# Performance work log

Measured on AMD Instinct MI355X. Metric: run time of the kernel, lower is better.

Reference implementation:

```python
import jax, jax.numpy as jnp
import numpy as np

N_HEAD, D_MODEL, D_HEAD = 16, 1024, 64
SEQ, BSZ = 2048, 4
LN_EPS = 1e-5
SCALE = 1.0 / D_HEAD ** 0.5


def layer_norm(x, gamma, beta):
    m = jnp.mean(x, axis=-1, keepdims=True)
    v = jnp.mean(jnp.square(x - m), axis=-1, keepdims=True)
    return (x - m) * jax.lax.rsqrt(v + LN_EPS) * gamma + beta


def setup_inputs() -> dict:
    key = jax.random.key(0)
    k1, k2, k3, k4, k5, k6 = jax.random.split(key, 6)
    h = jax.random.normal(k1, (SEQ, BSZ, D_MODEL), dtype=jnp.float32)
    attn_mask = jax.random.bernoulli(k2, 0.1, (SEQ, BSZ))
    s = 1.0 / np.sqrt(D_MODEL)
    Wq = jax.random.normal(k3, (D_MODEL, N_HEAD * D_HEAD), dtype=jnp.float32) * s
    Wkv = jax.random.normal(k4, (D_MODEL, 2 * N_HEAD * D_HEAD), dtype=jnp.float32) * s
    Wo = jax.random.normal(k5, (N_HEAD * D_HEAD, D_MODEL), dtype=jnp.float32) * s
    gamma = jnp.ones((D_MODEL,), dtype=jnp.float32)
    beta = jnp.zeros((D_MODEL,), dtype=jnp.float32)
    return {"h": h, "attn_mask": attn_mask, "Wq": Wq, "Wkv": Wkv,
            "Wo": Wo, "gamma": gamma, "beta": beta}


def reference(h, attn_mask, Wq, Wkv, Wo, gamma, beta):
    # h: [S, B, D]; post-LN variant (pre_lnorm=False), mems=None so c == h
    S, B, _ = h.shape
    head_q = (h @ Wq).reshape(S, B, N_HEAD, D_HEAD)
    kv = h @ Wkv
    head_k, head_v = jnp.split(kv, 2, axis=-1)
    head_k = head_k.reshape(S, B, N_HEAD, D_HEAD)
    head_v = head_v.reshape(S, B, N_HEAD, D_HEAD)
    # scores [qlen, klen, B, n]
    attn_score = jnp.einsum('ibnd,jbnd->ijbn', head_q, head_k) * SCALE
    # 2D mask [klen, B] broadcast as [1, klen, B, 1]
    attn_score = jnp.where(attn_mask[None, :, :, None], -jnp.inf, attn_score)
    attn_prob = jax.nn.softmax(attn_score, axis=1)
    attn_vec = jnp.einsum('ijbn,jbnd->ibnd', attn_prob, head_v)
    attn_vec = attn_vec.reshape(S, B, N_HEAD * D_HEAD)
    attn_out = attn_vec @ Wo
    return layer_norm(h + attn_out, gamma, beta)
```

## Files before the change

### kernel.cpp

```cpp
#include <hip/hip_runtime.h>
#include <stdint.h>

#define SEQ 2048
#define BSZ 4
#define NHEAD 16
#define DHEAD 64
#define DMODEL 1024
#define NHD (NHEAD * DHEAD)
#define KVSTR (2 * NHD)

typedef unsigned short u16;
typedef unsigned char u8;
typedef unsigned int u32;
typedef float v4f __attribute__((ext_vector_type(4)));
typedef short v8s __attribute__((ext_vector_type(8)));
typedef u32 v4u __attribute__((ext_vector_type(4)));
typedef u32 v2u __attribute__((ext_vector_type(2)));

#define MASK_NEG 30000.0f
#define BF16_ONES_PAIR 0x3F803F80u

__device__ __forceinline__ float bf2f(u16 h) { return __uint_as_float(((u32)h) << 16); }
__device__ __forceinline__ u16 f2bf(float f) {
  u32 u = __float_as_uint(f);
  return (u16)((u + 0x7fffu + ((u >> 16) & 1u)) >> 16);
}
__device__ __forceinline__ v4f v4f_zero() {
  v4f z; z[0] = 0.f; z[1] = 0.f; z[2] = 0.f; z[3] = 0.f; return z;
}
__device__ __forceinline__ bool is_bf16_mode(const u32* gprobe) {
  return *gprobe == BF16_ONES_PAIR;
}
__device__ __forceinline__ u32 pack_bf16_trunc(float a, float b) {
  return __builtin_amdgcn_perm(__float_as_uint(b), __float_as_uint(a), 0x07060302u);
}

typedef __attribute__((address_space(3))) u32 lds_u32_t;
typedef const __attribute__((address_space(1))) u32 g_u32_t;
__device__ __forceinline__ void async_cp16(const u16* gp, u16* lp) {
  __builtin_amdgcn_global_load_lds((g_u32_t*)gp, (lds_u32_t*)lp, 16, 0, 0);
}

__global__ __launch_bounds__(256) void cast_h(
    const void* __restrict__ src, const u32* __restrict__ gprobe,
    u16* __restrict__ dst) {
  bool bf = is_bf16_mode(gprobe);
  int i4 = blockIdx.x * 256 + threadIdx.x;
  if (bf) {
    ((v2u*)dst)[i4] = ((const v2u*)src)[i4];
  } else {
    v4f v = ((const v4f*)src)[i4];
    v2u o;
    o[0] = (u32)f2bf(v[0]) | ((u32)f2bf(v[1]) << 16);
    o[1] = (u32)f2bf(v[2]) | ((u32)f2bf(v[3]) << 16);
    ((v2u*)dst)[i4] = o;
  }
}

__global__ __launch_bounds__(256) void transpose_w3(
    const void* __restrict__ Wq, const void* __restrict__ Wkv,
    const void* __restrict__ Wo, const u32* __restrict__ gprobe,
    const u32* __restrict__ mraw,
    u16* __restrict__ WqT, u16* __restrict__ WkvT, u16* __restrict__ WoT,
    float* __restrict__ maskf) {
  int z = blockIdx.z;
  if (z == 3) {
    int flat = blockIdx.y * 64 + blockIdx.x;
    if (flat >= 32) return;
    bool int8mode = false;
    for (int i = 0; i < 64; ++i) {
      u32 v = mraw[i];
      if (v != 0u && v != 1u && v != 0x3F800000u) int8mode = true;
    }
    int idx = flat * 256 + threadIdx.x;
    int b = idx >> 11, j = idx & 2047;
    u32 val = int8mode ? (u32)((const u8*)mraw)[j * BSZ + b] : mraw[j * BSZ + b];
    maskf[idx] = val ? -MASK_NEG : 0.0f;
    return;
  }
  bool bf = is_bf16_mode(gprobe);
  int C = (z == 1) ? 2048 : 1024;
  if (blockIdx.x * 32 >= (unsigned)C) return;
  const void* src = (z == 0) ? Wq : (z == 1) ? Wkv : Wo;
  u16* outp = (z == 0) ? WqT : (z == 1) ? WkvT : WoT;
  __shared__ u16 tile[32][33];
  int c0 = blockIdx.x * 32, r0 = blockIdx.y * 32;
  int tx = threadIdx.x & 31, ty = threadIdx.x >> 5;
  if (bf) {
    const u16* in = (const u16*)src;
#pragma unroll
    for (int rr = 0; rr < 4; ++rr)
      tile[ty + rr * 8][tx] = in[(r0 + ty + rr * 8) * C + c0 + tx];
  } else {
    const float* in = (const float*)src;
#pragma unroll
    for (int rr = 0; rr < 4; ++rr)
      tile[ty + rr * 8][tx] = f2bf(in[(r0 + ty + rr * 8) * C + c0 + tx]);
  }
  __syncthreads();
#pragma unroll
  for (int rr = 0; rr < 4; ++rr)
    outp[(c0 + ty + rr * 8) * 1024 + r0 + tx] = tile[tx][ty + rr * 8];
}

__global__ __launch_bounds__(256) void build_vt(
    const u16* __restrict__ KV, u16* __restrict__ Vt) {
  __shared__ u16 tile[32][33];
  int bn = blockIdx.z;
  int b = bn >> 4, n = bn & 15;
  int s0 = blockIdx.x * 32, d0 = blockIdx.y * 32;
  int tx = threadIdx.x & 31, ty = threadIdx.x >> 5;
#pragma unroll
  for (int rr = 0; rr < 4; ++rr) {
    int s = s0 + ty + rr * 8;
    tile[ty + rr * 8][tx] = KV[(s * BSZ + b) * KVSTR + NHD + n * DHEAD + d0 + tx];
  }
  __syncthreads();
  const int ptx = ((tx >> 2) & 3) * 8 + ((tx >> 4) & 1) * 4 + (tx & 3);
#pragma unroll
  for (int rr = 0; rr < 4; ++rr) {
    int d = d0 + ty + rr * 8;
    Vt[bn * (DHEAD * SEQ) + d * SEQ + s0 + ptx] = tile[tx][ty + rr * 8];
  }
}

__global__ __launch_bounds__(256) void gemm_qkv(
    const u16* __restrict__ A, const u16* __restrict__ Bt,
    u16* __restrict__ Qm, u16* __restrict__ KVm) {
  const int K = 1024;
  __shared__ __align__(16) u16 As[2][128 * 32];
  __shared__ __align__(16) u16 Bs[2][128 * 32];
  const int tid = threadIdx.x;
  const int lane = tid & 63, w = tid >> 6;
  const int quad = lane >> 4, l16 = lane & 15;
  const int wm = w >> 1, wn = w & 1;
  const int flat = blockIdx.y * 24 + blockIdx.x;
  const int xcd = flat & 7, idx = flat >> 3;
  const int m0 = (idx / 3) * 128;
  const int n0 = (xcd * 3 + idx % 3) * 128;
  const int qsw = quad ^ ((l16 >> 1) & 3);

  const int c8 = ((tid & 3) ^ ((tid >> 3) & 3)) * 8;
  const u16* aA = A + (size_t)(m0 + (tid >> 2)) * K + c8;
  const u16* bB = Bt + (size_t)(n0 + (tid >> 2)) * K + c8;

#define QKV_STAGE(bi, kk)                                   \
  do {                                                      \
    async_cp16(aA + (kk), &As[bi][8 * tid]);                \
    async_cp16(aA + 64 * K + (kk), &As[bi][2048 + 8 * tid]);\
    async_cp16(bB + (kk), &Bs[bi][8 * tid]);                \
    async_cp16(bB + 64 * K + (kk), &Bs[bi][2048 + 8 * tid]);\
  } while (0)

  v4f acc[4][4];
#pragma unroll
  for (int i = 0; i < 4; ++i)
#pragma unroll
    for (int j = 0; j < 4; ++j) acc[i][j] = v4f_zero();

  QKV_STAGE(0, 0);
  asm volatile("s_waitcnt vmcnt(0)" ::: "memory");
  __syncthreads();

  for (int k0 = 0; k0 < K; k0 += 32) {
    const int cur = (k0 >> 5) & 1;
    if (k0 + 32 < K) QKV_STAGE(cur ^ 1, k0 + 32);
    const u16* AsC = As[cur];
    const u16* BsC = Bs[cur];
    v8s a[4], b[4];
#pragma unroll
    for (int i = 0; i < 4; ++i)
      a[i] = *(const v8s*)(AsC + (wm * 64 + i * 16 + l16) * 32 + qsw * 8);
#pragma unroll
    for (int j = 0; j < 4; ++j)
      b[j] = *(const v8s*)(BsC + (wn * 64 + j * 16 + l16) * 32 + qsw * 8);
#pragma unroll
    for (int i = 0; i < 4; ++i)
#pragma unroll
      for (int j = 0; j < 4; ++j)
        acc[i][j] = __builtin_amdgcn_mfma_f32_16x16x32_bf16(a[i], b[j], acc[i][j], 0, 0, 0);
    asm volatile("s_waitcnt vmcnt(0)" ::: "memory");
    __syncthreads();
  }
#undef QKV_STAGE
  u16* dst = (n0 < 1024) ? Qm : KVm;
  int stride = (n0 < 1024) ? 1024 : 2048;
  int coff = (n0 < 1024) ? n0 : n0 - 1024;
#pragma unroll
  for (int i = 0; i < 4; ++i)
#pragma unroll
    for (int j = 0; j < 4; ++j)
#pragma unroll
      for (int r = 0; r < 4; ++r) {
        int row = m0 + wm * 64 + i * 16 + quad * 4 + r;
        int col = coff + wn * 64 + j * 16 + l16;
        dst[(size_t)row * stride + col] = f2bf(acc[i][j][r]);
      }
}

__global__ __launch_bounds__(256) void gemm_bt(
    const u16* __restrict__ A, const u16* __restrict__ Bt,
    u16* __restrict__ Cb, float* __restrict__ Cf, int store_f32,
    int N, int K) {
  __shared__ __align__(16) u16 As[2][128 * 32];
  __shared__ __align__(16) u16 Bs[2][128 * 32];
  const int tid = threadIdx.x;
  const int lane = tid & 63, w = tid >> 6;
  const int quad = lane >> 4, l16 = lane & 15;
  const int wm = w >> 1, wn = w & 1;
  const int nbx = gridDim.x;
  const int flat = blockIdx.y * nbx + blockIdx.x;
  const int chunk = (nbx * gridDim.y) >> 3;
  const int logical = (flat & 7) * chunk + (flat >> 3);
  const int m0 = (logical / nbx) * 128, n0 = (logical % nbx) * 128;
  const int qsw = quad ^ ((l16 >> 1) & 3);

  const int c8 = ((tid & 3) ^ ((tid >> 3) & 3)) * 8;
  const u16* aA = A + (size_t)(m0 + (tid >> 2)) * K + c8;
  const u16* bB = Bt + (size_t)(n0 + (tid >> 2)) * K + c8;

#define BT_STAGE(bi, kk)                                    \
  do {                                                      \
    async_cp16(aA + (kk), &As[bi][8 * tid]);                \
    async_cp16(aA + 64 * K + (kk), &As[bi][2048 + 8 * tid]);\
    async_cp16(bB + (kk), &Bs[bi][8 * tid]);                \
    async_cp16(bB + 64 * K + (kk), &Bs[bi][2048 + 8 * tid]);\
  } while (0)

  v4f acc[4][4];
#pragma unroll
  for (int i = 0; i < 4; ++i)
#pragma unroll
    for (int j = 0; j < 4; ++j) acc[i][j] = v4f_zero();

  BT_STAGE(0, 0);
  asm volatile("s_waitcnt vmcnt(0)" ::: "memory");
  __syncthreads();

  for (int k0 = 0; k0 < K; k0 += 32) {
    const int cur = (k0 >> 5) & 1;
    if (k0 + 32 < K) BT_STAGE(cur ^ 1, k0 + 32);
    const u16* AsC = As[cur];
    const u16* BsC = Bs[cur];
    v8s a[4], b[4];
#pragma unroll
    for (int i = 0; i < 4; ++i)
      a[i] = *(const v8s*)(AsC + (wm * 64 + i * 16 + l16) * 32 + qsw * 8);
#pragma unroll
    for (int j = 0; j < 4; ++j)
      b[j] = *(const v8s*)(BsC + (wn * 64 + j * 16 + l16) * 32 + qsw * 8);
#pragma unroll
    for (int i = 0; i < 4; ++i)
#pragma unroll
      for (int j = 0; j < 4; ++j)
        acc[i][j] = __builtin_amdgcn_mfma_f32_16x16x32_bf16(a[i], b[j], acc[i][j], 0, 0, 0);
    asm volatile("s_waitcnt vmcnt(0)" ::: "memory");
    __syncthreads();
  }
#undef BT_STAGE
#pragma unroll
  for (int i = 0; i < 4; ++i)
#pragma unroll
    for (int j = 0; j < 4; ++j)
#pragma unroll
      for (int r = 0; r < 4; ++r) {
        int row = m0 + wm * 64 + i * 16 + quad * 4 + r;
        int col = n0 + wn * 64 + j * 16 + l16;
        if (store_f32) Cf[(size_t)row * N + col] = acc[i][j][r];
        else Cb[(size_t)row * N + col] = f2bf(acc[i][j][r]);
      }
}

__global__ __launch_bounds__(512, 4) void attn(
    const u16* __restrict__ Q, const u16* __restrict__ KV,
    const u16* __restrict__ Vt, const float* __restrict__ maskf,
    u16* __restrict__ AV) {
  __shared__ __align__(16) u16 Ks[2][2 * 64 * 32];
  __shared__ __align__(16) u16 Vs[2][2 * 64 * 32];

  const int tid = threadIdx.x;
  const int lane = tid & 63, w = tid >> 6;
  const int quad = lane >> 4, l16 = lane & 15;
  const int flat = blockIdx.y * 8 + blockIdx.x;
  const int logical = (flat & 7) * 64 + (flat >> 3);
  const int bn = logical >> 3;
  const int b = bn >> 4, n = bn & 15;
  const int q0 = (logical & 7) * 256 + w * 16;
  const int qsw = quad ^ ((l16 >> 1) & 3);

  const float SC = 0.125f * 1.44269504088896340736f;

  const int rl = (tid >> 2) & 63;
  const int half = tid >> 8;
  const int cks = (tid & 3) ^ ((tid >> 3) & 3);
  const u16* kb = KV + ((size_t)rl * BSZ + b) * KVSTR + n * DHEAD + half * 32 + cks * 8;
  const u16* vb = Vt + (size_t)bn * (DHEAD * SEQ) + (size_t)rl * SEQ + half * 32 + cks * 8;

#define STAGE_JT(bi, jtn)                                                  \
  do {                                                                     \
    async_cp16(kb + (size_t)(jtn) * (64 * BSZ * KVSTR), &Ks[bi][8 * tid]); \
    async_cp16(vb + (jtn) * 64,                         &Vs[bi][8 * tid]); \
  } while (0)

  v8s qf[2][2];
#pragma unroll
  for (int s = 0; s < 2; ++s)
#pragma unroll
    for (int c = 0; c < 2; ++c)
      qf[s][c] = *(const v8s*)(Q + ((size_t)(q0 + s * 128 + l16) * BSZ + b) * NHD +
                               n * DHEAD + c * 32 + quad * 8);

  v4f ot[2][4];
#pragma unroll
  for (int s = 0; s < 2; ++s)
#pragma unroll
    for (int d = 0; d < 4; ++d) ot[s][d] = v4f_zero();
  v4f lacc[2];
  lacc[0] = v4f_zero();
  lacc[1] = v4f_zero();
  union OU { v4u u; v8s v; } ones;
  ones.u[0] = BF16_ONES_PAIR; ones.u[1] = BF16_ONES_PAIR;
  ones.u[2] = BF16_ONES_PAIR; ones.u[3] = BF16_ONES_PAIR;

  const float* mrow = maskf + b * SEQ + quad * 4;

  STAGE_JT(0, 0);
  asm volatile("s_waitcnt vmcnt(0)" ::: "memory");
  __syncthreads();

  for (int jt = 0; jt < SEQ / 64; ++jt) {
    const int cur = jt & 1;
    if (jt + 1 < SEQ / 64) STAGE_JT(cur ^ 1, jt + 1);

    v4f mk[4];
#pragma unroll
    for (int t = 0; t < 4; ++t)
      mk[t] = *(const v4f*)(mrow + jt * 64 + t * 16);

    const u16* KsC = Ks[cur];
    const u16* VsC = Vs[cur];

    v4f st[2][4];
    __builtin_amdgcn_s_setprio(1);
#pragma unroll
    for (int t = 0; t < 4; ++t) {
      v8s kf0 = *(const v8s*)(KsC + (t * 16 + l16) * 32 + qsw * 8);
      v8s kf1 = *(const v8s*)(KsC + (2048 + (t * 16 + l16) * 32) + qsw * 8);
#pragma unroll
      for (int s = 0; s < 2; ++s) {
        v4f acc = __builtin_amdgcn_mfma_f32_16x16x32_bf16(kf0, qf[s][0], v4f_zero(), 0, 0, 0);
        st[s][t] = __builtin_amdgcn_mfma_f32_16x16x32_bf16(kf1, qf[s][1], acc, 0, 0, 0);
      }
    }
    __builtin_amdgcn_s_setprio(0);

    union PU { v4u u; v8s s; };
    PU pf[2][2];
#pragma unroll
    for (int s = 0; s < 2; ++s)
#pragma unroll
      for (int t = 0; t < 4; ++t) {
        v4f msk = mk[t];
        float p0 = __builtin_amdgcn_exp2f(fmaf(st[s][t][0], SC, msk[0]));
        float p1 = __builtin_amdgcn_exp2f(fmaf(st[s][t][1], SC, msk[1]));
        float p2 = __builtin_amdgcn_exp2f(fmaf(st[s][t][2], SC, msk[2]));
        float p3 = __builtin_amdgcn_exp2f(fmaf(st[s][t][3], SC, msk[3]));
        pf[s][t >> 1].u[(t & 1) * 2 + 0] = pack_bf16_trunc(p0, p1);
        pf[s][t >> 1].u[(t & 1) * 2 + 1] = pack_bf16_trunc(p2, p3);
      }

    __builtin_amdgcn_s_setprio(1);
#pragma unroll
    for (int tp = 0; tp < 2; ++tp) {
#pragma unroll
      for (int ds = 0; ds < 4; ++ds) {
        v8s vf = *(const v8s*)(VsC + tp * 2048 + (ds * 16 + l16) * 32 + qsw * 8);
#pragma unroll
        for (int s = 0; s < 2; ++s)
          ot[s][ds] = __builtin_amdgcn_mfma_f32_16x16x32_bf16(vf, pf[s][tp].s, ot[s][ds], 0, 0, 0);
      }
#pragma unroll
      for (int s = 0; s < 2; ++s)
        lacc[s] = __builtin_amdgcn_mfma_f32_16x16x32_bf16(ones.v, pf[s][tp].s, lacc[s], 0, 0, 0);
    }
    __builtin_amdgcn_s_setprio(0);

    asm volatile("s_waitcnt vmcnt(0)" ::: "memory");
    __syncthreads();
  }
#undef STAGE_JT

#pragma unroll
  for (int s = 0; s < 2; ++s) {
    float inv = 1.0f / fmaxf(lacc[s][0], 1e-30f);
#pragma unroll
    for (int ds = 0; ds < 4; ++ds)
#pragma unroll
      for (int r = 0; r < 4; ++r) {
        int d = ds * 16 + quad * 4 + r;
        AV[((size_t)(q0 + s * 128 + l16) * BSZ + b) * NHD + n * DHEAD + d] =
            f2bf(ot[s][ds][r] * inv);
      }
  }
}

__global__ __launch_bounds__(256) void add_ln(
    const void* __restrict__ h, const float* __restrict__ AO,
    const void* __restrict__ gamma, const void* __restrict__ beta,
    void* __restrict__ outp) {
  bool bf = is_bf16_mode((const u32*)gamma);
  const int row = blockIdx.x, tid = threadIdx.x;
  const int lane = tid & 63, w = tid >> 6;
  __shared__ float rs1[4], rs2[4];
  const int col = tid * 4;
  v4f av = *(const v4f*)(AO + (size_t)row * DMODEL + col);
  float x[4], g[4], be[4];
  if (bf) {
    v2u hv = ((const v2u*)h)[row * 256 + tid];
    x[0] = bf2f((u16)(hv[0] & 0xffff)) + av[0];
    x[1] = bf2f((u16)(hv[0] >> 16)) + av[1];
    x[2] = bf2f((u16)(hv[1] & 0xffff)) + av[2];
    x[3] = bf2f((u16)(hv[1] >> 16)) + av[3];
    v2u gv = ((const v2u*)gamma)[tid];
    v2u bv = ((const v2u*)beta)[tid];
    g[0] = bf2f((u16)(gv[0] & 0xffff)); g[1] = bf2f((u16)(gv[0] >> 16));
    g[2] = bf2f((u16)(gv[1] & 0xffff)); g[3] = bf2f((u16)(gv[1] >> 16));
    be[0] = bf2f((u16)(bv[0] & 0xffff)); be[1] = bf2f((u16)(bv[0] >> 16));
    be[2] = bf2f((u16)(bv[1] & 0xffff)); be[3] = bf2f((u16)(bv[1] >> 16));
  } else {
    v4f hv = ((const v4f*)h)[row * 256 + tid];
    x[0] = hv[0] + av[0]; x[1] = hv[1] + av[1];
    x[2] = hv[2] + av[2]; x[3] = hv[3] + av[3];
    v4f gv = ((const v4f*)gamma)[tid];
    v4f bv = ((const v4f*)beta)[tid];
    g[0] = gv[0]; g[1] = gv[1]; g[2] = gv[2]; g[3] = gv[3];
    be[0] = bv[0]; be[1] = bv[1]; be[2] = bv[2]; be[3] = bv[3];
  }
  float s1 = x[0] + x[1] + x[2] + x[3];
  float s2 = x[0] * x[0] + x[1] * x[1] + x[2] * x[2] + x[3] * x[3];
#pragma unroll
  for (int off = 1; off < 64; off <<= 1) {
    s1 += __shfl_xor(s1, off);
    s2 += __shfl_xor(s2, off);
  }
  if (lane == 0) { rs1[w] = s1; rs2[w] = s2; }
  __syncthreads();
  s1 = rs1[0] + rs1[1] + rs1[2] + rs1[3];
  s2 = rs2[0] + rs2[1] + rs2[2] + rs2[3];
  float mean = s1 * (1.0f / DMODEL);
  float var = s2 * (1.0f / DMODEL) - mean * mean;
  float rstd = rsqrtf(var + 1e-5f);
  float y0 = (x[0] - mean) * rstd * g[0] + be[0];
  float y1 = (x[1] - mean) * rstd * g[1] + be[1];
  float y2 = (x[2] - mean) * rstd * g[2] + be[2];
  float y3 = (x[3] - mean) * rstd * g[3] + be[3];
  if (bf) {
    v2u ov;
    ov[0] = (u32)f2bf(y0) | ((u32)f2bf(y1) << 16);
    ov[1] = (u32)f2bf(y2) | ((u32)f2bf(y3) << 16);
    ((v2u*)outp)[row * 256 + tid] = ov;
  } else {
    v4f ov; ov[0] = y0; ov[1] = y1; ov[2] = y2; ov[3] = y3;
    ((v4f*)outp)[row * 256 + tid] = ov;
  }
}

extern "C" void kernel_launch(void* const* d_in, const int* in_sizes, int n_in,
                              void* d_out, int out_size, void* d_ws, size_t ws_size,
                              hipStream_t stream) {
  const void* h    = d_in[0];
  const u32* mask  = (const u32*)d_in[1];
  const void* Wq   = d_in[2];
  const void* Wkv  = d_in[3];
  const void* Wo   = d_in[4];
  const void* gamma = d_in[5];
  const void* beta  = d_in[6];
  const u32* gprobe = (const u32*)gamma;

  char* ws = (char*)d_ws;
  const size_t MB = 1 << 20;
  u16* hb      = (u16*)(ws + 0 * MB);
  u16* Vtm     = (u16*)(ws + 0 * MB);
  u16* KVm     = (u16*)(ws + 16 * MB);
  float* AOm   = (float*)(ws + 16 * MB);
  u16* WqT     = (u16*)(ws + 48 * MB);
  u16* WkvT    = (u16*)(ws + 50 * MB);
  u16* WoT     = (u16*)(ws + 54 * MB);
  float* maskf = (float*)(ws + 56 * MB);
  u16* Qm      = (u16*)d_out;

  cast_h<<<dim3(8192), 256, 0, stream>>>(h, gprobe, hb);
  transpose_w3<<<dim3(64, 32, 4), 256, 0, stream>>>(Wq, Wkv, Wo, gprobe, mask,
                                                    WqT, WkvT, WoT, maskf);

  gemm_qkv<<<dim3(24, 64), 256, 0, stream>>>(hb, WqT, Qm, KVm);

  build_vt<<<dim3(64, 2, 64), 256, 0, stream>>>(KVm, Vtm);

  attn<<<dim3(8, 64), 512, 0, stream>>>(Qm, KVm, Vtm, maskf, Qm);

  gemm_bt<<<dim3(8, 64), 256, 0, stream>>>(Qm, WoT, nullptr, AOm, 1, 1024, 1024);
  add_ln<<<dim3(8192), 256, 0, stream>>>(h, AOm, gamma, beta, d_out);
}
```

Baseline: 296.5 us.

## Triple-buffer LDS stages in projection GEMMs with partial vmcnt waits

Both the QKV projection GEMM and the generic B-transposed GEMM go from double to triple buffering of shared-memory tiles. Each iteration prefetches two K-steps ahead and waits only until the older stage has landed (vmcnt(4)) instead of draining all loads, using a raw s_barrier. The aim is to hide global-to-LDS latency behind the MFMA work. In exchange, shared memory per block grows to 48KB, which may lower occupancy, and the raw barrier relies on the hand-counted vmcnt being correct.

```diff
diff --git a/kernel.cpp b/kernel.cpp
--- a/kernel.cpp
+++ b/kernel.cpp
@@ -128,8 +128,8 @@
     const u16* __restrict__ A, const u16* __restrict__ Bt,
     u16* __restrict__ Qm, u16* __restrict__ KVm) {
   const int K = 1024;
-  __shared__ __align__(16) u16 As[2][128 * 32];
-  __shared__ __align__(16) u16 Bs[2][128 * 32];
+  __shared__ __align__(16) u16 As[3][128 * 32];
+  __shared__ __align__(16) u16 Bs[3][128 * 32];
   const int tid = threadIdx.x;
   const int lane = tid & 63, w = tid >> 6;
   const int quad = lane >> 4, l16 = lane & 15;
@@ -159,12 +159,18 @@
     for (int j = 0; j < 4; ++j) acc[i][j] = v4f_zero();
 
   QKV_STAGE(0, 0);
-  asm volatile("s_waitcnt vmcnt(0)" ::: "memory");
-  __syncthreads();
-
+  QKV_STAGE(1, 32);
+  asm volatile("s_waitcnt vmcnt(4)" ::: "memory");
+  __builtin_amdgcn_s_barrier();
+  asm volatile("" ::: "memory");
+
+  int cur = 0;
   for (int k0 = 0; k0 < K; k0 += 32) {
-    const int cur = (k0 >> 5) & 1;
-    if (k0 + 32 < K) QKV_STAGE(cur ^ 1, k0 + 32);
+    const bool stg = (k0 + 64 < K);
+    if (stg) {
+      int nb = cur + 2; if (nb >= 3) nb -= 3;
+      QKV_STAGE(nb, k0 + 64);
+    }
     const u16* AsC = As[cur];
     const u16* BsC = Bs[cur];
     v8s a[4], b[4];
@@ -179,8 +185,11 @@
 #pragma unroll
       for (int j = 0; j < 4; ++j)
         acc[i][j] = __builtin_amdgcn_mfma_f32_16x16x32_bf16(a[i], b[j], acc[i][j], 0, 0, 0);
-    asm volatile("s_waitcnt vmcnt(0)" ::: "memory");
-    __syncthreads();
+    if (stg) asm volatile("s_waitcnt vmcnt(4)" ::: "memory");
+    else     asm volatile("s_waitcnt vmcnt(0)" ::: "memory");
+    __builtin_amdgcn_s_barrier();
+    asm volatile("" ::: "memory");
+    cur = (cur + 1 >= 3) ? 0 : cur + 1;
   }
 #undef QKV_STAGE
   u16* dst = (n0 < 1024) ? Qm : KVm;
@@ -202,8 +211,8 @@
     const u16* __restrict__ A, const u16* __restrict__ Bt,
     u16* __restrict__ Cb, float* __restrict__ Cf, int store_f32,
     int N, int K) {
-  __shared__ __align__(16) u16 As[2][128 * 32];
-  __shared__ __align__(16) u16 Bs[2][128 * 32];
+  __shared__ __align__(16) u16 As[3][128 * 32];
+  __shared__ __align__(16) u16 Bs[3][128 * 32];
   const int tid = threadIdx.x;
   const int lane = tid & 63, w = tid >> 6;
   const int quad = lane >> 4, l16 = lane & 15;
@@ -234,12 +243,18 @@
     for (int j = 0; j < 4; ++j) acc[i][j] = v4f_zero();
 
   BT_STAGE(0, 0);
-  asm volatile("s_waitcnt vmcnt(0)" ::: "memory");
-  __syncthreads();
-
+  BT_STAGE(1, 32);
+  asm volatile("s_waitcnt vmcnt(4)" ::: "memory");
+  __builtin_amdgcn_s_barrier();
+  asm volatile("" ::: "memory");
+
+  int cur = 0;
   for (int k0 = 0; k0 < K; k0 += 32) {
-    const int cur = (k0 >> 5) & 1;
-    if (k0 + 32 < K) BT_STAGE(cur ^ 1, k0 + 32);
+    const bool stg = (k0 + 64 < K);
+    if (stg) {
+      int nb = cur + 2; if (nb >= 3) nb -= 3;
+      BT_STAGE(nb, k0 + 64);
+    }
     const u16* AsC = As[cur];
     const u16* BsC = Bs[cur];
     v8s a[4], b[4];
@@ -254,8 +269,11 @@
 #pragma unroll
       for (int j = 0; j < 4; ++j)
         acc[i][j] = __builtin_amdgcn_mfma_f32_16x16x32_bf16(a[i], b[j], acc[i][j], 0, 0, 0);
-    asm volatile("s_waitcnt vmcnt(0)" ::: "memory");
-    __syncthreads();
+    if (stg) asm volatile("s_waitcnt vmcnt(4)" ::: "memory");
+    else     asm volatile("s_waitcnt vmcnt(0)" ::: "memory");
+    __builtin_amdgcn_s_barrier();
+    asm volatile("" ::: "memory");
+    cur = (cur + 1 >= 3) ? 0 : cur + 1;
   }
 #undef BT_STAGE
 #pragma unroll
```

Measured after the change: 296.6 us. About the same (+0.0%).
